# Kernel optimization log

Measured on AMD Instinct MI355X. Metric: run time of the kernel, lower is better.

The kernel has to match this reference:

```python
import jax, jax.numpy as jnp
import numpy as np

B, S, H, NH, L, MLP_MULT = 4, 1024, 1024, 16, 2, 4
DK = H // NH
EPS = 1e-5


def setup_inputs() -> dict:
    key = jax.random.key(0)
    ks = jax.random.split(key, 8)
    p = lambda k, shape: jax.random.normal(k, shape, dtype=jnp.float32) * 0.02
    return {
        'hidden_states': jax.random.normal(ks[0], (B, S, H), dtype=jnp.float32),
        'attn_w': p(ks[1], (L, H, 3 * H)),
        'attn_b': jnp.zeros((L, 3 * H), jnp.float32),
        'proj_w': p(ks[2], (L, H, H)),
        'proj_b': jnp.zeros((L, H), jnp.float32),
        'fc_w': p(ks[3], (L, H, MLP_MULT * H)),
        'fc_b': jnp.zeros((L, MLP_MULT * H), jnp.float32),
        'fc2_w': p(ks[4], (L, MLP_MULT * H, H)),
        'fc2_b': jnp.zeros((L, H), jnp.float32),
        'ln1_g': jnp.ones((L, H), jnp.float32),
        'ln1_b': jnp.zeros((L, H), jnp.float32),
        'ln2_g': jnp.ones((L, H), jnp.float32),
        'ln2_b': jnp.zeros((L, H), jnp.float32),
        'position_ids': jnp.arange(S, dtype=jnp.int32),
    }


def _ln(x, g, b):
    m = jnp.mean(x, axis=-1, keepdims=True)
    v = jnp.var(x, axis=-1, keepdims=True)
    return (x - m) * jax.lax.rsqrt(v + EPS) * g + b


def _rotate_half(x):
    x1, x2 = jnp.split(x, 2, axis=-1)
    return jnp.concatenate((-x2, x1), axis=-1)


def _forward(hidden_states, attn_w, attn_b, proj_w, proj_b, fc_w, fc_b,
             fc2_w, fc2_b, ln1_g, ln1_b, ln2_g, ln2_b, position_ids):
    # rotary tables (fp32 math, as in RotaryEmbedding.forward)
    inv_freq = 1.0 / (10000.0 ** (jnp.arange(0, DK, 2, dtype=jnp.float32) / DK))
    freqs = position_ids.astype(jnp.float32)[:, None] * inv_freq[None, :]  # [S, DK/2]
    emb = jnp.concatenate((freqs, freqs), axis=-1)                          # [S, DK]
    cos = jnp.cos(emb)[None, None]  # [1,1,S,DK]
    sin = jnp.sin(emb)[None, None]
    causal = jnp.tril(jnp.ones((S, S), dtype=bool))
    neg = jnp.finfo(jnp.float32).min
    scale = 1.0 / np.sqrt(DK).astype(np.float32)

    h = hidden_states
    for i in range(L):
        # attention block
        x = _ln(h, ln1_g[i], ln1_b[i])
        qkv = x @ attn_w[i] + attn_b[i]                  # Conv1D c_attn
        q, k, v = jnp.split(qkv, 3, axis=-1)
        heads = lambda t: t.reshape(B, S, NH, DK).transpose(0, 2, 1, 3)
        q, k, v = heads(q), heads(k), heads(v)           # [B,NH,S,DK]
        q = q * cos + _rotate_half(q) * sin
        k = k * cos + _rotate_half(k) * sin
        # fp32 QK^T (baddbmm with alpha=scale, beta=0)
        w = jnp.einsum('bhqd,bhkd->bhqk', q.astype(jnp.float32),
                       k.astype(jnp.float32)) * scale    # [B,NH,S,S]
        w = jnp.where(causal, w, neg)
        w = jax.nn.softmax(w, axis=-1).astype(v.dtype)   # attn dropout is identity (eval)
        a = jnp.einsum('bhqk,bhkd->bhqd', w, v)
        a = a.transpose(0, 2, 1, 3).reshape(B, S, H)     # merge_heads
        h = h + (a @ proj_w[i] + proj_b[i])              # c_proj + residual
        # MLP block (gelu_new == tanh-approx gelu)
        x = _ln(h, ln2_g[i], ln2_b[i])
        mid = jax.nn.gelu(x @ fc_w[i] + fc_b[i], approximate=True)
        h = h + (mid @ fc2_w[i] + fc2_b[i])
    return h


def reference(hidden_states, attn_w, attn_b, proj_w, proj_b, fc_w, fc_b,
              fc2_w, fc2_b, ln1_g, ln1_b, ln2_g, ln2_b, position_ids):
    return _forward(hidden_states, attn_w, attn_b, proj_w, proj_b, fc_w, fc_b,
                    fc2_w, fc2_b, ln1_g, ln1_b, ln2_g, ln2_b, position_ids)
```

## Files before the change

### kernel.cpp

```cpp
#include <hip/hip_runtime.h>

#define B_ 4
#define S_ 1024
#define H_ 1024
#define NH_ 16
#define DK_ 64
#define MLPH_ 4096
#define EPS_ 1e-5f

typedef __attribute__((ext_vector_type(8))) short short8_t;
typedef __attribute__((ext_vector_type(8))) unsigned short ushort8_t;
typedef __attribute__((ext_vector_type(4))) float f32x4;

__device__ __forceinline__ unsigned short f2bf(float f) {
  unsigned int u = __float_as_uint(f);
  u = u + 0x7fffu + ((u >> 16) & 1u);
  return (unsigned short)(u >> 16);
}
__device__ __forceinline__ float bf2f(unsigned short b) {
  return __uint_as_float(((unsigned int)b) << 16);
}

__device__ __forceinline__ void gload16(const void* g, void* l) {
  typedef const __attribute__((address_space(1))) unsigned int GU;
  typedef __attribute__((address_space(3))) unsigned int LU;
  __builtin_amdgcn_global_load_lds((GU*)(size_t)g, (LU*)(unsigned int)(size_t)l, 16, 0, 0);
}

__device__ __forceinline__ float gelu_tanh(float x) {
  float y = 1.5957691216057308f * (x + 0.044715f * x * x * x);
  return x / (1.0f + __expf(-y));
}

__global__ __launch_bounds__(256) void wconv(const float* __restrict__ src0,
                                             unsigned short* __restrict__ dst0,
                                             int K, int N) {
  __shared__ float t[32][33];
  const float* src = src0 + (size_t)blockIdx.z * K * N;
  unsigned short* dst = dst0 + (size_t)blockIdx.z * N * K;
  int n0 = blockIdx.x * 32, k0 = blockIdx.y * 32;
  int tid = threadIdx.x;
  int r = tid >> 3, c = (tid & 7) * 4;
  const float* s = src + (size_t)(k0 + r) * N + n0 + c;
  float4 v = *(const float4*)s;
  t[r][c] = v.x; t[r][c + 1] = v.y; t[r][c + 2] = v.z; t[r][c + 3] = v.w;
  __syncthreads();
  ushort4 o;
  o.x = f2bf(t[c + 0][r]); o.y = f2bf(t[c + 1][r]);
  o.z = f2bf(t[c + 2][r]); o.w = f2bf(t[c + 3][r]);
  *(ushort4*)(dst + (size_t)(n0 + r) * K + k0 + c) = o;
}

__global__ __launch_bounds__(256) void ln_kernel(const float* __restrict__ x,
                                                 const float* __restrict__ g,
                                                 const float* __restrict__ b,
                                                 unsigned short* __restrict__ y) {
  int row = blockIdx.x, tid = threadIdx.x;
  const float* xp = x + (size_t)row * H_;
  float4 v = *((const float4*)xp + tid);
  float s  = v.x + v.y + v.z + v.w;
  float s2 = v.x * v.x + v.y * v.y + v.z * v.z + v.w * v.w;
  #pragma unroll
  for (int o = 1; o < 64; o <<= 1) {
    s  += __shfl_xor(s, o, 64);
    s2 += __shfl_xor(s2, o, 64);
  }
  __shared__ float r1[4], r2[4];
  if ((tid & 63) == 0) { r1[tid >> 6] = s; r2[tid >> 6] = s2; }
  __syncthreads();
  s  = r1[0] + r1[1] + r1[2] + r1[3];
  s2 = r2[0] + r2[1] + r2[2] + r2[3];
  float mean = s * (1.0f / H_);
  float var  = s2 * (1.0f / H_) - mean * mean;
  float inv  = rsqrtf(var + EPS_);
  float4 gv = *((const float4*)g + tid);
  float4 bv = *((const float4*)b + tid);
  ushort4 o;
  o.x = f2bf((v.x - mean) * inv * gv.x + bv.x);
  o.y = f2bf((v.y - mean) * inv * gv.y + bv.y);
  o.z = f2bf((v.z - mean) * inv * gv.z + bv.z);
  o.w = f2bf((v.w - mean) * inv * gv.w + bv.w);
  *(ushort4*)(y + (size_t)row * H_ + tid * 4) = o;
}

template <int MODE, int NT>
__global__ __launch_bounds__(256) void gemm_mfma(
    const unsigned short* __restrict__ A, const unsigned short* __restrict__ Bt,
    const float* __restrict__ bias, const float* __restrict__ resid,
    void* __restrict__ outp, int M, int N, int K, const int* __restrict__ pos) {
  constexpr int BN = NT * 32;
  constexpr int CB = BN / 32;
  __shared__ __align__(16) unsigned short As[2][128 * 64];
  __shared__ __align__(16) unsigned short Bs[2][BN * 64];
  int tid = threadIdx.x;
  int w = tid >> 6, lane = tid & 63;
  int gx = gridDim.x;
  int nwg = gx * gridDim.y;
  int bid = blockIdx.y * gx + blockIdx.x;
  int cpx = nwg >> 3;
  int swz = (bid & 7) * cpx + (bid >> 3);
  int m0 = (swz / gx) * 128, n0 = (swz % gx) * BN;
  int wr = w >> 1, wc = w & 1;
  int fr = lane & 15, kg = lane >> 4;
  f32x4 acc[4][NT];
  #pragma unroll
  for (int m = 0; m < 4; m++)
    #pragma unroll
    for (int n = 0; n < NT; n++) {
      acc[m][n][0] = 0.f; acc[m][n][1] = 0.f; acc[m][n][2] = 0.f; acc[m][n][3] = 0.f;
    }
  int srow = lane >> 3;
  int scol = ((lane & 7) ^ srow) * 8;
  const unsigned short* Ap = A  + (size_t)(m0 + w * 32 + srow) * K + scol;
  const unsigned short* Bp = Bt + (size_t)(n0 + w * (8 * CB) + srow) * K + scol;
  int sx = (fr & 7);
  int nk = K >> 6;
  {
    char* AsB = (char*)As[0] + w * 4096;
    char* BsB = (char*)Bs[0] + w * CB * 1024;
    #pragma unroll
    for (int i = 0; i < 4; i++) gload16(Ap + (size_t)i * 8 * K, AsB + i * 1024);
    #pragma unroll
    for (int i = 0; i < CB; i++) gload16(Bp + (size_t)i * 8 * K, BsB + i * 1024);
  }
  __syncthreads();
  for (int t = 0; t < nk; t++) {
    int cur = t & 1;
    if (t + 1 < nk) {
      const unsigned short* Ap2 = Ap + (size_t)(t + 1) * 64;
      const unsigned short* Bp2 = Bp + (size_t)(t + 1) * 64;
      char* AsB = (char*)As[cur ^ 1] + w * 4096;
      char* BsB = (char*)Bs[cur ^ 1] + w * CB * 1024;
      #pragma unroll
      for (int i = 0; i < 4; i++) gload16(Ap2 + (size_t)i * 8 * K, AsB + i * 1024);
      #pragma unroll
      for (int i = 0; i < CB; i++) gload16(Bp2 + (size_t)i * 8 * K, BsB + i * 1024);
    }
    #pragma unroll
    for (int kk = 0; kk < 2; kk++) {
      int slot = ((kk * 4 + kg) ^ sx) << 4;
      short8_t af[4], bfr[NT];
      #pragma unroll
      for (int m = 0; m < 4; m++)
        af[m] = *(const short8_t*)((char*)As[cur] + (wr * 64 + m * 16 + fr) * 128 + slot);
      #pragma unroll
      for (int n = 0; n < NT; n++)
        bfr[n] = *(const short8_t*)((char*)Bs[cur] + (wc * (NT * 16) + n * 16 + fr) * 128 + slot);
      #pragma unroll
      for (int m = 0; m < 4; m++)
        #pragma unroll
        for (int n = 0; n < NT; n++)
          acc[m][n] = __builtin_amdgcn_mfma_f32_16x16x32_bf16(af[m], bfr[n], acc[m][n], 0, 0, 0);
    }
    __syncthreads();
  }

  if (MODE == 3) {
    int seg = n0 >> 10;
    if (seg < 2) {
      #pragma unroll
      for (int n = 0; n < 2; n++) {
        int col0 = n0 + wc * 64 + n * 16 + fr;
        int d2 = n * 16 + fr;
        float invf = __expf(-0.2878231366242557f * (float)d2);
        float bv0 = bias[col0], bv2 = bias[col0 + 32];
        #pragma unroll
        for (int m = 0; m < 4; m++) {
          int row = m0 + wr * 64 + m * 16 + kg * 4;
          #pragma unroll
          for (int r = 0; r < 4; r++) {
            int s = (row + r) & (S_ - 1);
            float th = (float)pos[s] * invf;
            float sn, cs;
            __sincosf(th, &sn, &cs);
            float a0 = acc[m][n][r] + bv0;
            float a2 = acc[m][n + 2][r] + bv2;
            size_t base = (size_t)(row + r) * N;
            ((unsigned short*)outp)[base + col0]      = f2bf(a0 * cs - a2 * sn);
            ((unsigned short*)outp)[base + col0 + 32] = f2bf(a2 * cs + a0 * sn);
          }
        }
      }
    } else {
      #pragma unroll
      for (int n = 0; n < NT; n++) {
        int col = n0 + wc * (NT * 16) + n * 16 + fr;
        float bv = bias[col];
        #pragma unroll
        for (int m = 0; m < 4; m++) {
          int row = m0 + wr * 64 + m * 16 + kg * 4;
          #pragma unroll
          for (int r = 0; r < 4; r++)
            ((unsigned short*)outp)[(size_t)(row + r) * N + col] = f2bf(acc[m][n][r] + bv);
        }
      }
    }
    return;
  }
  #pragma unroll
  for (int n = 0; n < NT; n++) {
    int col = n0 + wc * (NT * 16) + n * 16 + fr;
    float bv = bias[col];
    #pragma unroll
    for (int m = 0; m < 4; m++) {
      int row = m0 + wr * 64 + m * 16 + kg * 4;
      #pragma unroll
      for (int r = 0; r < 4; r++) {
        float v = acc[m][n][r] + bv;
        size_t idx = (size_t)(row + r) * N + col;
        if (MODE == 2)      ((float*)outp)[idx] = resid[idx] + v;
        else if (MODE == 1) ((unsigned short*)outp)[idx] = f2bf(gelu_tanh(v));
        else                ((unsigned short*)outp)[idx] = f2bf(v);
      }
    }
  }
}

__global__ __launch_bounds__(256) void attn7(const unsigned short* __restrict__ qkv,
                                             unsigned short* __restrict__ aout) {
  __shared__ __align__(16) unsigned short Ks[2][64 * 64];
  __shared__ __align__(16) unsigned short Vt[2][64 * 64];
  __shared__ __align__(16) unsigned short Ps[4][2][16 * 64];
  const float SCL2 = 0.18033688011112443f;
  const float THR2 = 11.541560327111708f;
  int tid = threadIdx.x;
  int w = tid >> 6, lane = tid & 63;
  int fr = lane & 15, kg = lane >> 4;
  int qt = (int)gridDim.x - 1 - (int)blockIdx.x;
  int q0 = qt * 128;
  int head = blockIdx.y, b = blockIdx.z;
  const unsigned short* base = qkv + ((size_t)b * S_) * 3072 + head * 64;

  short8_t qa0[2], qa1[2];
  #pragma unroll
  for (int g = 0; g < 2; g++) {
    const unsigned short* qp = base + (size_t)(q0 + w * 32 + g * 16 + fr) * 3072 + kg * 8;
    qa0[g] = *(const short8_t*)qp;
    qa1[g] = *(const short8_t*)(qp + 32);
  }

  f32x4 acc[2][4];
  float mrun[2], lrun[2];
  #pragma unroll
  for (int g = 0; g < 2; g++) {
    mrun[g] = -3.0e38f; lrun[g] = 0.f;
    #pragma unroll
    for (int n = 0; n < 4; n++) {
      acc[g][n][0] = 0.f; acc[g][n][1] = 0.f; acc[g][n][2] = 0.f; acc[g][n][3] = 0.f;
    }
  }

  int skv = lane;
  int sd0 = w * 16;
  int qg[2];
  qg[0] = q0 + w * 32 + fr;
  qg[1] = qg[0] + 16;

  const unsigned short* kp0 = base + 1024 + (size_t)skv * 3072 + sd0;
  short8_t ka = *(const short8_t*)kp0;
  short8_t kb = *(const short8_t*)(kp0 + 8);
  short8_t va = *(const short8_t*)(kp0 + 1024);
  short8_t vb = *(const short8_t*)(kp0 + 1032);

  int ntiles = 2 * qt + 2;
  for (int t = 0; t < ntiles; t++) {
    int cur = t & 1;
    {
      unsigned kbyte = skv * 128 + sd0 * 2;
      unsigned ksw = (skv & 7) << 4;
      *(short8_t*)((char*)Ks[cur] + (kbyte ^ ksw)) = ka;
      *(short8_t*)((char*)Ks[cur] + ((kbyte + 16) ^ ksw)) = kb;
      #pragma unroll
      for (int j = 0; j < 8; j++) {
        int d0 = sd0 + j, d1 = sd0 + 8 + j;
        *(unsigned short*)((char*)Vt[cur] + ((d0 * 128 + skv * 2) ^ ((d0 & 7) << 4))) = (unsigned short)va[j];
        *(unsigned short*)((char*)Vt[cur] + ((d1 * 128 + skv * 2) ^ ((d1 & 7) << 4))) = (unsigned short)vb[j];
      }
    }
    if (t + 1 < ntiles) {
      const unsigned short* kp = base + 1024 + (size_t)((t + 1) * 64 + skv) * 3072 + sd0;
      ka = *(const short8_t*)kp;
      kb = *(const short8_t*)(kp + 8);
      va = *(const short8_t*)(kp + 1024);
      vb = *(const short8_t*)(kp + 1032);
    }
    __syncthreads();
    short8_t b0[4], b1[4], v0[4], v1[4];
    #pragma unroll
    for (int n = 0; n < 4; n++) {
      int kvrow = n * 16 + fr;
      unsigned sw = (kvrow & 7) << 4;
      b0[n] = *(const short8_t*)((char*)Ks[cur] + ((kvrow * 128 + kg * 16) ^ sw));
      b1[n] = *(const short8_t*)((char*)Ks[cur] + ((kvrow * 128 + 64 + kg * 16) ^ sw));
    }
    #pragma unroll
    for (int n = 0; n < 4; n++) {
      int d = n * 16 + fr;
      unsigned sw = (d & 7) << 4;
      v0[n] = *(const short8_t*)((char*)Vt[cur] + ((d * 128 + kg * 16) ^ sw));
      v1[n] = *(const short8_t*)((char*)Vt[cur] + ((d * 128 + 64 + kg * 16) ^ sw));
    }
    f32x4 st[2][4];
    __builtin_amdgcn_s_setprio(1);
    #pragma unroll
    for (int g = 0; g < 2; g++)
      #pragma unroll
      for (int n = 0; n < 4; n++) {
        f32x4 z; z[0] = 0.f; z[1] = 0.f; z[2] = 0.f; z[3] = 0.f;
        z = __builtin_amdgcn_mfma_f32_16x16x32_bf16(b0[n], qa0[g], z, 0, 0, 0);
        z = __builtin_amdgcn_mfma_f32_16x16x32_bf16(b1[n], qa1[g], z, 0, 0, 0);
        st[g][n] = z;
      }
    __builtin_amdgcn_s_setprio(0);
    bool diag = (t >= 2 * qt);
    float pmax[2];
    #pragma unroll
    for (int g = 0; g < 2; g++) {
      float rm = -3.0e38f;
      #pragma unroll
      for (int n = 0; n < 4; n++)
        #pragma unroll
        for (int j = 0; j < 4; j++) {
          float sv = st[g][n][j] * SCL2;
          if (diag && (t * 64 + n * 16 + kg * 4 + j > qg[g])) sv = -1.0e30f;
          st[g][n][j] = sv;
          rm = fmaxf(rm, sv);
        }
      pmax[g] = rm;
    }
    bool need = (pmax[0] > mrun[0] + THR2) | (pmax[1] > mrun[1] + THR2);
    if (__any(need)) {
      #pragma unroll
      for (int g = 0; g < 2; g++) {
        float rm = pmax[g];
        rm = fmaxf(rm, __shfl_xor(rm, 16, 64));
        rm = fmaxf(rm, __shfl_xor(rm, 32, 64));
        float mn = fmaxf(mrun[g], rm);
        float sc = exp2f(mrun[g] - mn);
        mrun[g] = mn;
        lrun[g] *= sc;
        #pragma unroll
        for (int n = 0; n < 4; n++) {
          acc[g][n][0] *= sc; acc[g][n][1] *= sc; acc[g][n][2] *= sc; acc[g][n][3] *= sc;
        }
      }
    }
    #pragma unroll
    for (int g = 0; g < 2; g++) {
      float ls = 0.f;
      #pragma unroll
      for (int n = 0; n < 4; n++) {
        float e0 = exp2f(st[g][n][0] - mrun[g]);
        float e1 = exp2f(st[g][n][1] - mrun[g]);
        float e2 = exp2f(st[g][n][2] - mrun[g]);
        float e3 = exp2f(st[g][n][3] - mrun[g]);
        ls += (e0 + e1) + (e2 + e3);
        unsigned lo, hi;
        asm("v_cvt_pk_bf16_f32 %0, %1, %2" : "=v"(lo) : "v"(e0), "v"(e1));
        asm("v_cvt_pk_bf16_f32 %0, %1, %2" : "=v"(hi) : "v"(e2), "v"(e3));
        uint2 pk; pk.x = lo; pk.y = hi;
        *(uint2*)((char*)Ps[w][g] + ((fr * 128 + n * 32 + kg * 8) ^ ((fr & 7) << 4))) = pk;
      }
      lrun[g] += ls;
    }
    asm volatile("s_waitcnt lgkmcnt(0)" ::: "memory");
    unsigned psw = (fr & 7) << 4;
    short8_t pa0[2], pa1[2];
    #pragma unroll
    for (int g = 0; g < 2; g++) {
      pa0[g] = *(const short8_t*)((char*)Ps[w][g] + ((fr * 128 + kg * 16) ^ psw));
      pa1[g] = *(const short8_t*)((char*)Ps[w][g] + ((fr * 128 + 64 + kg * 16) ^ psw));
    }
    __builtin_amdgcn_s_setprio(1);
    #pragma unroll
    for (int n = 0; n < 4; n++)
      #pragma unroll
      for (int g = 0; g < 2; g++) {
        acc[g][n] = __builtin_amdgcn_mfma_f32_16x16x32_bf16(v0[n], pa0[g], acc[g][n], 0, 0, 0);
        acc[g][n] = __builtin_amdgcn_mfma_f32_16x16x32_bf16(v1[n], pa1[g], acc[g][n], 0, 0, 0);
      }
    __builtin_amdgcn_s_setprio(0);
  }
  #pragma unroll
  for (int g = 0; g < 2; g++) {
    float ls = lrun[g];
    ls += __shfl_xor(ls, 16, 64);
    ls += __shfl_xor(ls, 32, 64);
    float inv = 1.0f / ls;
    size_t row = (size_t)b * S_ + q0 + w * 32 + g * 16 + fr;
    unsigned short* op = aout + row * H_ + head * 64 + kg * 4;
    #pragma unroll
    for (int n = 0; n < 4; n++) {
      ushort4 o;
      o.x = f2bf(acc[g][n][0] * inv);
      o.y = f2bf(acc[g][n][1] * inv);
      o.z = f2bf(acc[g][n][2] * inv);
      o.w = f2bf(acc[g][n][3] * inv);
      *(ushort4*)(op + n * 16) = o;
    }
  }
}

extern "C" void kernel_launch(void* const* d_in, const int* in_sizes, int n_in,
                              void* d_out, int out_size, void* d_ws, size_t ws_size,
                              hipStream_t stream) {
  const float* hs     = (const float*)d_in[0];
  const float* attn_w = (const float*)d_in[1];
  const float* attn_b = (const float*)d_in[2];
  const float* proj_w = (const float*)d_in[3];
  const float* proj_b = (const float*)d_in[4];
  const float* fc_w   = (const float*)d_in[5];
  const float* fc_b   = (const float*)d_in[6];
  const float* fc2_w  = (const float*)d_in[7];
  const float* fc2_b  = (const float*)d_in[8];
  const float* ln1_g  = (const float*)d_in[9];
  const float* ln1_b  = (const float*)d_in[10];
  const float* ln2_g  = (const float*)d_in[11];
  const float* ln2_b  = (const float*)d_in[12];
  const int*   pos    = (const int*)d_in[13];

  float* hres = (float*)d_out;
  const size_t rows = (size_t)B_ * S_;

  unsigned short* wQ    = (unsigned short*)d_ws;
  unsigned short* wP    = wQ  + (size_t)2 * 3072 * 1024;
  unsigned short* wF1   = wP  + (size_t)2 * 1024 * 1024;
  unsigned short* wF2   = wF1 + (size_t)2 * 4096 * 1024;
  unsigned short* xbf   = wF2 + (size_t)2 * 1024 * 4096;
  unsigned short* qkvbf = xbf + rows * H_;
  unsigned short* midbf = qkvbf + rows * 3 * H_;
  unsigned short* aoutbf= midbf + rows * MLPH_;

  hipMemcpyAsync(hres, hs, rows * H_ * sizeof(float), hipMemcpyDeviceToDevice, stream);

  wconv<<<dim3(96, 32, 2), 256, 0, stream>>>(attn_w, wQ, 1024, 3072);
  wconv<<<dim3(32, 32, 2), 256, 0, stream>>>(proj_w, wP, 1024, 1024);
  wconv<<<dim3(128, 32, 2), 256, 0, stream>>>(fc_w, wF1, 1024, 4096);
  wconv<<<dim3(32, 128, 2), 256, 0, stream>>>(fc2_w, wF2, 4096, 1024);

  for (int l = 0; l < 2; l++) {
    ln_kernel<<<rows, 256, 0, stream>>>(hres, ln1_g + l * H_, ln1_b + l * H_, xbf);
    gemm_mfma<3, 4><<<dim3(24, 32), 256, 0, stream>>>(
        xbf, wQ + (size_t)l * 3072 * 1024, attn_b + (size_t)l * 3072, nullptr,
        qkvbf, 4096, 3072, 1024, pos);
    attn7<<<dim3(8, 16, 4), 256, 0, stream>>>(qkvbf, aoutbf);
    gemm_mfma<2, 2><<<dim3(16, 32), 256, 0, stream>>>(
        aoutbf, wP + (size_t)l * 1024 * 1024, proj_b + (size_t)l * 1024, hres,
        hres, 4096, 1024, 1024, nullptr);
    ln_kernel<<<rows, 256, 0, stream>>>(hres, ln2_g + l * H_, ln2_b + l * H_, xbf);
    gemm_mfma<1, 4><<<dim3(32, 32), 256, 0, stream>>>(
        xbf, wF1 + (size_t)l * 4096 * 1024, fc_b + (size_t)l * 4096, nullptr,
        midbf, 4096, 4096, 1024, nullptr);
    gemm_mfma<2, 2><<<dim3(16, 32), 256, 0, stream>>>(
        midbf, wF2 + (size_t)l * 1024 * 4096, fc2_b + (size_t)l * 1024, hres,
        hres, 4096, 1024, 4096, nullptr);
  }
}
```

Measured before the change: 445.6 us.

## Halve attention query tile, balance causal work with ordering, drop residual memcpy

The attention kernel now processes 64 query rows per block (one 16-row group per wave) instead of 128, doubling the grid to 1024 blocks. A remapped block index orders query tiles in four phases (descending, ascending, mid-range) so long and short causal rows interleave across the GPU. The initial device-to-device copy of the hidden states is removed: the first layer reads LN input and the residual directly from the input buffer. Smaller tiles mean each K/V tile loaded into shared memory is reused by fewer query rows, so there is more K/V traffic per unit of compute.

New measurement: 406.6 us. 8.7% less time.

```diff
diff --git a/kernel.cpp b/kernel.cpp
--- a/kernel.cpp
+++ b/kernel.cpp
@@ -216,45 +216,42 @@
   }
 }
 
-__global__ __launch_bounds__(256) void attn7(const unsigned short* __restrict__ qkv,
+__global__ __launch_bounds__(256) void attn9(const unsigned short* __restrict__ qkv,
                                              unsigned short* __restrict__ aout) {
   __shared__ __align__(16) unsigned short Ks[2][64 * 64];
   __shared__ __align__(16) unsigned short Vt[2][64 * 64];
-  __shared__ __align__(16) unsigned short Ps[4][2][16 * 64];
+  __shared__ __align__(16) unsigned short Ps[4][16 * 64];
   const float SCL2 = 0.18033688011112443f;
   const float THR2 = 11.541560327111708f;
   int tid = threadIdx.x;
   int w = tid >> 6, lane = tid & 63;
   int fr = lane & 15, kg = lane >> 4;
-  int qt = (int)gridDim.x - 1 - (int)blockIdx.x;
-  int q0 = qt * 128;
-  int head = blockIdx.y, b = blockIdx.z;
+  int lid = ((blockIdx.z << 4) + blockIdx.y) * 16 + blockIdx.x;
+  int phase = lid >> 8, s256 = lid & 255;
+  int i = s256 >> 6, combo = s256 & 63;
+  int qt;
+  if (phase == 0)      qt = 15 - i;
+  else if (phase == 1) qt = i;
+  else if (phase == 2) qt = 11 - i;
+  else                 qt = 4 + i;
+  int head = combo & 15, b = combo >> 4;
+  int q0 = qt * 64;
   const unsigned short* base = qkv + ((size_t)b * S_) * 3072 + head * 64;
 
-  short8_t qa0[2], qa1[2];
+  const unsigned short* qp = base + (size_t)(q0 + w * 16 + fr) * 3072 + kg * 8;
+  short8_t qa0 = *(const short8_t*)qp;
+  short8_t qa1 = *(const short8_t*)(qp + 32);
+
+  f32x4 acc[4];
+  float mrun = -3.0e38f, lrun = 0.f;
   #pragma unroll
-  for (int g = 0; g < 2; g++) {
-    const unsigned short* qp = base + (size_t)(q0 + w * 32 + g * 16 + fr) * 3072 + kg * 8;
-    qa0[g] = *(const short8_t*)qp;
-    qa1[g] = *(const short8_t*)(qp + 32);
-  }
-
-  f32x4 acc[2][4];
-  float mrun[2], lrun[2];
-  #pragma unroll
-  for (int g = 0; g < 2; g++) {
-    mrun[g] = -3.0e38f; lrun[g] = 0.f;
-    #pragma unroll
-    for (int n = 0; n < 4; n++) {
-      acc[g][n][0] = 0.f; acc[g][n][1] = 0.f; acc[g][n][2] = 0.f; acc[g][n][3] = 0.f;
-    }
+  for (int n = 0; n < 4; n++) {
+    acc[n][0] = 0.f; acc[n][1] = 0.f; acc[n][2] = 0.f; acc[n][3] = 0.f;
   }
 
   int skv = lane;
   int sd0 = w * 16;
-  int qg[2];
-  qg[0] = q0 + w * 32 + fr;
-  qg[1] = qg[0] + 16;
+  int qrow = q0 + w * 16 + fr;
 
   const unsigned short* kp0 = base + 1024 + (size_t)skv * 3072 + sd0;
   short8_t ka = *(const short8_t*)kp0;
@@ -262,7 +259,7 @@
   short8_t va = *(const short8_t*)(kp0 + 1024);
   short8_t vb = *(const short8_t*)(kp0 + 1032);
 
-  int ntiles = 2 * qt + 2;
+  int ntiles = qt + 1;
   for (int t = 0; t < ntiles; t++) {
     int cur = t & 1;
     {
@@ -300,102 +297,82 @@
       v0[n] = *(const short8_t*)((char*)Vt[cur] + ((d * 128 + kg * 16) ^ sw));
       v1[n] = *(const short8_t*)((char*)Vt[cur] + ((d * 128 + 64 + kg * 16) ^ sw));
     }
-    f32x4 st[2][4];
+    f32x4 st[4];
     __builtin_amdgcn_s_setprio(1);
     #pragma unroll
-    for (int g = 0; g < 2; g++)
+    for (int n = 0; n < 4; n++) {
+      f32x4 z; z[0] = 0.f; z[1] = 0.f; z[2] = 0.f; z[3] = 0.f;
+      z = __builtin_amdgcn_mfma_f32_16x16x32_bf16(b0[n], qa0, z, 0, 0, 0);
+      z = __builtin_amdgcn_mfma_f32_16x16x32_bf16(b1[n], qa1, z, 0, 0, 0);
+      st[n] = z;
+    }
+    __builtin_amdgcn_s_setprio(0);
+    bool diag = (t == qt);
+    float rm = -3.0e38f;
+    #pragma unroll
+    for (int n = 0; n < 4; n++)
+      #pragma unroll
+      for (int j = 0; j < 4; j++) {
+        float sv = st[n][j] * SCL2;
+        if (diag && (t * 64 + n * 16 + kg * 4 + j > qrow)) sv = -1.0e30f;
+        st[n][j] = sv;
+        rm = fmaxf(rm, sv);
+      }
+    if (__any(rm > mrun + THR2)) {
+      rm = fmaxf(rm, __shfl_xor(rm, 16, 64));
+      rm = fmaxf(rm, __shfl_xor(rm, 32, 64));
+      float mn = fmaxf(mrun, rm);
+      float sc = exp2f(mrun - mn);
+      mrun = mn;
+      lrun *= sc;
       #pragma unroll
       for (int n = 0; n < 4; n++) {
-        f32x4 z; z[0] = 0.f; z[1] = 0.f; z[2] = 0.f; z[3] = 0.f;
-        z = __builtin_amdgcn_mfma_f32_16x16x32_bf16(b0[n], qa0[g], z, 0, 0, 0);
-        z = __builtin_amdgcn_mfma_f32_16x16x32_bf16(b1[n], qa1[g], z, 0, 0, 0);
-        st[g][n] = z;
-      }
-    __builtin_amdgcn_s_setprio(0);
-    bool diag = (t >= 2 * qt);
-    float pmax[2];
-    #pragma unroll
-    for (int g = 0; g < 2; g++) {
-      float rm = -3.0e38f;
-      #pragma unroll
-      for (int n = 0; n < 4; n++)
-        #pragma unroll
-        for (int j = 0; j < 4; j++) {
-          float sv = st[g][n][j] * SCL2;
-          if (diag && (t * 64 + n * 16 + kg * 4 + j > qg[g])) sv = -1.0e30f;
-          st[g][n][j] = sv;
-          rm = fmaxf(rm, sv);
-        }
-      pmax[g] = rm;
-    }
-    bool need = (pmax[0] > mrun[0] + THR2) | (pmax[1] > mrun[1] + THR2);
-    if (__any(need)) {
-      #pragma unroll
-      for (int g = 0; g < 2; g++) {
-        float rm = pmax[g];
-        rm = fmaxf(rm, __shfl_xor(rm, 16, 64));
-        rm = fmaxf(rm, __shfl_xor(rm, 32, 64));
-        float mn = fmaxf(mrun[g], rm);
-        float sc = exp2f(mrun[g] - mn);
-        mrun[g] = mn;
-        lrun[g] *= sc;
-        #pragma unroll
-        for (int n = 0; n < 4; n++) {
-          acc[g][n][0] *= sc; acc[g][n][1] *= sc; acc[g][n][2] *= sc; acc[g][n][3] *= sc;
-        }
-      }
-    }
-    #pragma unroll
-    for (int g = 0; g < 2; g++) {
+        acc[n][0] *= sc; acc[n][1] *= sc; acc[n][2] *= sc; acc[n][3] *= sc;
+      }
+    }
+    {
       float ls = 0.f;
       #pragma unroll
       for (int n = 0; n < 4; n++) {
-        float e0 = exp2f(st[g][n][0] - mrun[g]);
-        float e1 = exp2f(st[g][n][1] - mrun[g]);
-        float e2 = exp2f(st[g][n][2] - mrun[g]);
-        float e3 = exp2f(st[g][n][3] - mrun[g]);
+        float e0 = exp2f(st[n][0] - mrun);
+        float e1 = exp2f(st[n][1] - mrun);
+        float e2 = exp2f(st[n][2] - mrun);
+        float e3 = exp2f(st[n][3] - mrun);
         ls += (e0 + e1) + (e2 + e3);
         unsigned lo, hi;
         asm("v_cvt_pk_bf16_f32 %0, %1, %2" : "=v"(lo) : "v"(e0), "v"(e1));
         asm("v_cvt_pk_bf16_f32 %0, %1, %2" : "=v"(hi) : "v"(e2), "v"(e3));
         uint2 pk; pk.x = lo; pk.y = hi;
-        *(uint2*)((char*)Ps[w][g] + ((fr * 128 + n * 32 + kg * 8) ^ ((fr & 7) << 4))) = pk;
-      }
-      lrun[g] += ls;
+        *(uint2*)((char*)Ps[w] + ((fr * 128 + n * 32 + kg * 8) ^ ((fr & 7) << 4))) = pk;
+      }
+      lrun += ls;
     }
     asm volatile("s_waitcnt lgkmcnt(0)" ::: "memory");
     unsigned psw = (fr & 7) << 4;
-    short8_t pa0[2], pa1[2];
-    #pragma unroll
-    for (int g = 0; g < 2; g++) {
-      pa0[g] = *(const short8_t*)((char*)Ps[w][g] + ((fr * 128 + kg * 16) ^ psw));
-      pa1[g] = *(const short8_t*)((char*)Ps[w][g] + ((fr * 128 + 64 + kg * 16) ^ psw));
-    }
+    short8_t pa0 = *(const short8_t*)((char*)Ps[w] + ((fr * 128 + kg * 16) ^ psw));
+    short8_t pa1 = *(const short8_t*)((char*)Ps[w] + ((fr * 128 + 64 + kg * 16) ^ psw));
     __builtin_amdgcn_s_setprio(1);
     #pragma unroll
-    for (int n = 0; n < 4; n++)
-      #pragma unroll
-      for (int g = 0; g < 2; g++) {
-        acc[g][n] = __builtin_amdgcn_mfma_f32_16x16x32_bf16(v0[n], pa0[g], acc[g][n], 0, 0, 0);
-        acc[g][n] = __builtin_amdgcn_mfma_f32_16x16x32_bf16(v1[n], pa1[g], acc[g][n], 0, 0, 0);
-      }
+    for (int n = 0; n < 4; n++) {
+      acc[n] = __builtin_amdgcn_mfma_f32_16x16x32_bf16(v0[n], pa0, acc[n], 0, 0, 0);
+      acc[n] = __builtin_amdgcn_mfma_f32_16x16x32_bf16(v1[n], pa1, acc[n], 0, 0, 0);
+    }
     __builtin_amdgcn_s_setprio(0);
   }
-  #pragma unroll
-  for (int g = 0; g < 2; g++) {
-    float ls = lrun[g];
+  {
+    float ls = lrun;
     ls += __shfl_xor(ls, 16, 64);
     ls += __shfl_xor(ls, 32, 64);
     float inv = 1.0f / ls;
-    size_t row = (size_t)b * S_ + q0 + w * 32 + g * 16 + fr;
+    size_t row = (size_t)b * S_ + q0 + w * 16 + fr;
     unsigned short* op = aout + row * H_ + head * 64 + kg * 4;
     #pragma unroll
     for (int n = 0; n < 4; n++) {
       ushort4 o;
-      o.x = f2bf(acc[g][n][0] * inv);
-      o.y = f2bf(acc[g][n][1] * inv);
-      o.z = f2bf(acc[g][n][2] * inv);
-      o.w = f2bf(acc[g][n][3] * inv);
+      o.x = f2bf(acc[n][0] * inv);
+      o.y = f2bf(acc[n][1] * inv);
+      o.z = f2bf(acc[n][2] * inv);
+      o.w = f2bf(acc[n][3] * inv);
       *(ushort4*)(op + n * 16) = o;
     }
   }
@@ -431,21 +408,20 @@
   unsigned short* midbf = qkvbf + rows * 3 * H_;
   unsigned short* aoutbf= midbf + rows * MLPH_;
 
-  hipMemcpyAsync(hres, hs, rows * H_ * sizeof(float), hipMemcpyDeviceToDevice, stream);
-
   wconv<<<dim3(96, 32, 2), 256, 0, stream>>>(attn_w, wQ, 1024, 3072);
   wconv<<<dim3(32, 32, 2), 256, 0, stream>>>(proj_w, wP, 1024, 1024);
   wconv<<<dim3(128, 32, 2), 256, 0, stream>>>(fc_w, wF1, 1024, 4096);
   wconv<<<dim3(32, 128, 2), 256, 0, stream>>>(fc2_w, wF2, 4096, 1024);
 
   for (int l = 0; l < 2; l++) {
-    ln_kernel<<<rows, 256, 0, stream>>>(hres, ln1_g + l * H_, ln1_b + l * H_, xbf);
+    const float* hin = (l == 0) ? hs : hres;
+    ln_kernel<<<rows, 256, 0, stream>>>(hin, ln1_g + l * H_, ln1_b + l * H_, xbf);
     gemm_mfma<3, 4><<<dim3(24, 32), 256, 0, stream>>>(
         xbf, wQ + (size_t)l * 3072 * 1024, attn_b + (size_t)l * 3072, nullptr,
         qkvbf, 4096, 3072, 1024, pos);
-    attn7<<<dim3(8, 16, 4), 256, 0, stream>>>(qkvbf, aoutbf);
+    attn9<<<dim3(16, 16, 4), 256, 0, stream>>>(qkvbf, aoutbf);
     gemm_mfma<2, 2><<<dim3(16, 32), 256, 0, stream>>>(
-        aoutbf, wP + (size_t)l * 1024 * 1024, proj_b + (size_t)l * 1024, hres,
+        aoutbf, wP + (size_t)l * 1024 * 1024, proj_b + (size_t)l * 1024, hin,
         hres, 4096, 1024, 1024, nullptr);
     ln_kernel<<<rows, 256, 0, stream>>>(hres, ln2_g + l * H_, ln2_b + l * H_, xbf);
     gemm_mfma<1, 4><<<dim3(32, 32), 256, 0, stream>>>(
```
